# Kernel tuning notes

Measured on AMD Instinct MI355X. Metric: run time of the kernel, lower is better.

## Reference

```python
import jax, jax.numpy as jnp
import numpy as np

TOPK = 5

def _l2norm(x, axis):
    n = jnp.sqrt(jnp.sum(x * x, axis=axis, keepdims=True))
    return x / jnp.maximum(n, 1e-12)

def _conv_block(x, w, b, g, beta):
    # Conv2d(k=3, stride=2, pad=1) + BatchNorm (train-mode batch stats) + ReLU + AvgPool2d(3,1,pad=1)
    x = jax.lax.conv_general_dilated(x, w, (2, 2), ((1, 1), (1, 1)),
                                     dimension_numbers=('NCHW', 'OIHW', 'NCHW'))
    x = x + b[None, :, None, None]
    mean = jnp.mean(x, axis=(0, 2, 3), keepdims=True)
    var = jnp.mean((x - mean) ** 2, axis=(0, 2, 3), keepdims=True)
    x = (x - mean) * jax.lax.rsqrt(var + 1e-5) * g[None, :, None, None] + beta[None, :, None, None]
    x = jax.nn.relu(x)
    # AvgPool2d default count_include_pad=True -> always divide by 9
    x = jax.lax.reduce_window(x, 0.0, jax.lax.add, (1, 1, 3, 3), (1, 1, 1, 1),
                              ((0, 0), (0, 0), (1, 1), (1, 1))) / 9.0
    return x

def _encode(x, params):
    x = x[:, None]  # B,1,T,D
    for (w, b, g, beta) in params:
        x = _conv_block(x, w, b, g, beta)
    return jnp.mean(x, axis=(2, 3))  # AdaptiveAvgPool2d(1) + flatten

def setup_inputs() -> dict:
    key = jax.random.key(0)
    ks = jax.random.split(key, 8)
    B, T, D = 128, 1024, 128
    dim, capQ, refD = 128, 2048, 2304
    inp = {}
    inp['feats'] = jax.random.normal(ks[0], (B, 2, T, D), jnp.float32)
    inp['ref_feats'] = jax.random.normal(ks[1], (B, refD), jnp.float32)
    inp['indices'] = jax.random.randint(ks[2], (B,), 0, 10000)
    mq = jax.random.normal(ks[3], (dim, capQ), jnp.float32)
    inp['MoCoQueue'] = mq / jnp.maximum(jnp.linalg.norm(mq, axis=0, keepdims=True), 1e-12)
    rq = jax.random.normal(ks[4], (refD, capQ), jnp.float32)
    inp['RefQueue'] = rq / jnp.maximum(jnp.linalg.norm(rq, axis=0, keepdims=True), 1e-12)
    inp['IndexQueue'] = jax.random.randint(ks[5], (capQ,), 0, 10000).astype(jnp.float32)
    chans = [1, 4, 16, 64, 128]
    pk = jax.random.split(ks[6], 4)
    for i in range(4):
        ci, co = chans[i], chans[i + 1]
        inp['w%d' % (i + 1)] = jax.random.normal(pk[i], (co, ci, 3, 3), jnp.float32) * 0.1
        inp['b%d' % (i + 1)] = jnp.zeros((co,), jnp.float32)
        inp['g%d' % (i + 1)] = jnp.ones((co,), jnp.float32)
        inp['be%d' % (i + 1)] = jnp.zeros((co,), jnp.float32)
    return inp

def reference(feats, ref_feats, indices, MoCoQueue, RefQueue, IndexQueue,
              w1, b1, g1, be1, w2, b2, g2, be2, w3, b3, g3, be3, w4, b4, g4, be4):
    params = [(w1, b1, g1, be1), (w2, b2, g2, be2), (w3, b3, g3, be3), (w4, b4, g4, be4)]
    q = _l2norm(_encode(feats[:, 1], params), 1)                      # B,dim
    k = jax.lax.stop_gradient(_l2norm(_encode(feats[:, 0], params), 1))
    ref = _l2norm(ref_feats, 1)                                       # B,2304
    B = q.shape[0]
    score_pos = jnp.sum(q * k, axis=1, keepdims=True)                 # B,1
    score_neg = q @ jax.lax.stop_gradient(MoCoQueue)                  # B,capQ
    mask = indices[:, None].astype(IndexQueue.dtype) == IndexQueue[None, :]  # B,capQ bool
    # queue_full=True branch: topk over reference queue similarities + scatter reweighting
    score_ref = ref @ jax.lax.stop_gradient(RefQueue)                 # B,capQ
    masked = jnp.where(mask, -jnp.inf, score_ref)
    _, idx = jax.lax.top_k(masked, TOPK)                              # B,topK
    score_ref2 = jnp.where(mask, 1.0, score_ref)
    rows = jnp.arange(B)[:, None]
    weighted = jnp.full_like(score_neg, -1.0).at[rows, idx].set(1.0)
    mask_f = mask.astype(jnp.float32).at[rows, idx].set(1.0)
    score_neg = score_neg * score_ref2 * weighted
    score = jnp.concatenate([score_pos, score_neg], axis=1)           # B,1+capQ
    mask_out = jnp.concatenate([jnp.ones((B, 1), jnp.float32), mask_f], axis=1)
    return score, mask_out
```

## Files before the change

kernel.cpp:

```cpp
#include <hip/hip_runtime.h>


#define NIMG 128
typedef __attribute__((ext_vector_type(8))) short bf16x8;
typedef __attribute__((ext_vector_type(4))) float f32x4;
typedef __attribute__((ext_vector_type(4))) unsigned int u32x4;
typedef unsigned long long ull;

__device__ __forceinline__ unsigned short f2bf(float f) {
  unsigned u = __float_as_uint(f);
  unsigned r = (u + 0x7fffu + ((u >> 16) & 1u)) >> 16;
  return (unsigned short)r;
}
__device__ __forceinline__ float bf2f(unsigned short u) {
  return __uint_as_float((unsigned)u << 16);
}

__global__ __launch_bounds__(256) void wtr4_k(
    const float* __restrict__ w2, const float* __restrict__ w3,
    const float* __restrict__ w4, unsigned short* __restrict__ wb2,
    unsigned short* __restrict__ wb3, unsigned short* __restrict__ wb4) {
  const int i = blockIdx.x * 256 + threadIdx.x;
  if (i < 16 * 64) {
    int co = i / 64, k = i % 64;
    int tap = k >> 2, ci = k & 3;
    float v = (k < 36) ? w2[co * 36 + ci * 9 + tap] : 0.f;
    wb2[i] = f2bf(v);
  }
  if (i < 64 * 160) {
    int co = i / 160, k = i % 160;
    int tap = k >> 4, ci = k & 15;
    float v = (k < 144) ? w3[co * 144 + ci * 9 + tap] : 0.f;
    wb3[i] = f2bf(v);
  }
  if (i < 128 * 576) {
    int co = i / 576, k = i % 576;
    int tap = k / 64, ci = k & 63;
    wb4[i] = f2bf(w4[co * 576 + ci * 9 + tap]);
  }
}

__device__ __forceinline__ void l1row(const float* __restrict__ ib, int ih,
                                      int w0i, float* r) {
  if (ih < 0) {
#pragma unroll
    for (int q = 0; q < 9; ++q) r[q] = 0.f;
    return;
  }
  const float* rp = ib + ih * 128 + 2 * w0i;
  const float4 a = *(const float4*)rp;
  const float4 b = *(const float4*)(rp + 4);
  r[0] = (w0i > 0) ? rp[-1] : 0.f;
  r[1] = a.x; r[2] = a.y; r[3] = a.z; r[4] = a.w;
  r[5] = b.x; r[6] = b.y; r[7] = b.z; r[8] = b.w;
}

__global__ __launch_bounds__(256, 4) void conv1s_k(const float* __restrict__ feats,
    const float* __restrict__ w1, const float* __restrict__ b1,
    unsigned short* __restrict__ y, float* __restrict__ part1,
    float* __restrict__ part2) {
  constexpr int TH = 2;
  const int tid = threadIdx.x;
  const int lw = tid & 15, grp = tid >> 4;
  const int h0 = (blockIdx.x * 16 + grp) * TH;
  const int pn = blockIdx.z;
  const int p = pn >> 7, n = pn & 127;
  const int sel = (p == 0) ? 1 : 0;
  const float* ib = feats + (size_t)(n * 2 + sel) * 131072;
  const int w0i = lw * 4;

  float wgt[36];
#pragma unroll
  for (int t = 0; t < 36; ++t) wgt[t] = w1[t];
  float bv[4];
#pragma unroll
  for (int c = 0; c < 4; ++c) bv[c] = b1[c];

  float r[5][9];
#pragma unroll
  for (int j = 0; j < 5; ++j) l1row(ib, 2 * h0 - 1 + j, w0i, r[j]);

  float s1[4] = {0.f, 0.f, 0.f, 0.f}, s2[4] = {0.f, 0.f, 0.f, 0.f};
#pragma unroll
  for (int t = 0; t < TH; ++t) {
    const int h = h0 + t;
    const float* r0 = r[2 * t];
    const float* r1 = r[2 * t + 1];
    const float* r2 = r[2 * t + 2];
#pragma unroll
    for (int co = 0; co < 4; ++co) {
      unsigned short ob[4];
#pragma unroll
      for (int i = 0; i < 4; ++i) {
        float v = bv[co];
#pragma unroll
        for (int kw = 0; kw < 3; ++kw) {
          v = fmaf(wgt[co * 9 + kw],     r0[2 * i + kw], v);
          v = fmaf(wgt[co * 9 + 3 + kw], r1[2 * i + kw], v);
          v = fmaf(wgt[co * 9 + 6 + kw], r2[2 * i + kw], v);
        }
        ob[i] = f2bf(v);
        s1[co] += v; s2[co] += v * v;
      }
      const ull o = (ull)ob[0] | ((ull)ob[1] << 16) | ((ull)ob[2] << 32)
                  | ((ull)ob[3] << 48);
      *(ull*)(y + (((size_t)pn * 4 + co) * 512 + h) * 64 + w0i) = o;
    }
  }
  __shared__ float ws1[4][4], ws2[4][4];
  const int lane = tid & 63, wid = tid >> 6;
#pragma unroll
  for (int co = 0; co < 4; ++co) {
#pragma unroll
    for (int m = 32; m >= 1; m >>= 1) {
      s1[co] += __shfl_xor(s1[co], m);
      s2[co] += __shfl_xor(s2[co], m);
    }
    if (lane == 0) { ws1[wid][co] = s1[co]; ws2[wid][co] = s2[co]; }
  }
  __syncthreads();
  if (tid < 4) {
    const float t1 = ws1[0][tid] + ws1[1][tid] + ws1[2][tid] + ws1[3][tid];
    const float t2 = ws2[0][tid] + ws2[1][tid] + ws2[2][tid] + ws2[3][tid];
    const int nblk = gridDim.x * 128;
    const int blk = (pn & 127) * gridDim.x + blockIdx.x;
    part1[(size_t)(p * 4 + tid) * nblk + blk] = t1;
    part2[(size_t)(p * 4 + tid) * nblk + blk] = t2;
  }
}

__device__ __forceinline__ bf16x8 ld16z(const unsigned short* p, bool ok) {
  u32x4 v = *(const u32x4*)p;
  if (!ok) v = (u32x4){0u, 0u, 0u, 0u};
  union { u32x4 a; bf16x8 b; } u; u.a = v; return u.b;
}

template<int Cin, int H, int W, int M, int SPB, int KP, int WCO, int WSP,
         int Cout, int MSPLIT, int WAVES>
__global__ __launch_bounds__(256, WAVES) void cgemmr_k(
    const unsigned short* __restrict__ x,
    const unsigned short* __restrict__ wb,
    const float* __restrict__ bias, unsigned short* __restrict__ y,
    float* __restrict__ part1, float* __restrict__ part2) {
  constexpr int Ho = H / 2, Wo = W / 2, HWout = Ho * Wo;
  constexpr int lgWo = (Wo == 8 ? 3 : (Wo == 16 ? 4 : 5));
  constexpr int lgCin = (Cin == 4 ? 2 : (Cin == 16 ? 4 : 6));
  constexpr int MB = M / MSPLIT;
  constexpr int MT = WCO / 16, NT = WSP / 16, KS = KP / 32;
  constexpr int NWN = SPB / WSP;
  __shared__ float ss1[MB], ss2[MB];
  const int tid = threadIdx.x;
  const int pnl = blockIdx.y;
  const int p = pnl >> 7;
  const int spc = blockIdx.x / MSPLIT;
  const int mc = blockIdx.x - spc * MSPLIT;
  const int sp0 = spc * SPB;
  const int m0 = mc * MB;
  const int lane = tid & 63, wid = tid >> 6;
  const int wm = wid / NWN, wn = wid - wm * NWN;
  const int l15 = lane & 15, lg = lane >> 4;
  const unsigned short* xb = x + (size_t)pnl * Cin * (H * W);

  for (int i = tid; i < MB; i += 256) { ss1[i] = 0.f; ss2[i] = 0.f; }
  __syncthreads();

  int ihb[NT], iwb[NT];
#pragma unroll
  for (int nt = 0; nt < NT; ++nt) {
    const int sp = sp0 + wn * WSP + nt * 16 + l15;
    ihb[nt] = 2 * (sp >> lgWo) - 1;
    iwb[nt] = 2 * (sp & (Wo - 1)) - 1;
  }

  f32x4 acc[MT][NT];
#pragma unroll
  for (int mt = 0; mt < MT; ++mt)
#pragma unroll
    for (int nt = 0; nt < NT; ++nt) acc[mt][nt] = (f32x4){0.f, 0.f, 0.f, 0.f};

#pragma unroll
  for (int ks = 0; ks < KS; ++ks) {
    const int kbase = ks * 32 + lg * 8;
    bf16x8 af[MT];
#pragma unroll
    for (int mt = 0; mt < MT; ++mt)
      af[mt] = *(const bf16x8*)(wb + (size_t)(m0 + wm * WCO + mt * 16 + l15) * KP
                                + kbase);
    bf16x8 bfr[NT];
#pragma unroll
    for (int nt = 0; nt < NT; ++nt) {
      if constexpr (Cin >= 8) {
        const int tap = kbase >> lgCin;
        const int ci0 = kbase & (Cin - 1);
        const int kh = tap / 3, kw = tap - kh * 3;
        const int ih = ihb[nt] + kh, iw = iwb[nt] + kw;
        const bool ok = (tap < 9) & ((unsigned)ih < (unsigned)H)
                      & ((unsigned)iw < (unsigned)W);
        const int off = ok ? ((ih * W + iw) * Cin + ci0) : 0;
        bfr[nt] = ld16z(xb + off, ok);
      } else {
        ull hv[2];
#pragma unroll
        for (int hh = 0; hh < 2; ++hh) {
          const int tap = (kbase >> 2) + hh;
          const int kh = tap / 3, kw = tap - kh * 3;
          const int ih = ihb[nt] + kh, iw = iwb[nt] + kw;
          const bool ok = (tap < 9) & ((unsigned)ih < (unsigned)H)
                        & ((unsigned)iw < (unsigned)W);
          const int off = ok ? ((ih * W + iw) * 4) : 0;
          const ull v = *(const ull*)(xb + off);
          hv[hh] = ok ? v : 0ull;
        }
        union { ull u[2]; bf16x8 b; } uu;
        uu.u[0] = hv[0]; uu.u[1] = hv[1];
        bfr[nt] = uu.b;
      }
    }
#pragma unroll
    for (int mt = 0; mt < MT; ++mt)
#pragma unroll
      for (int nt = 0; nt < NT; ++nt)
        acc[mt][nt] = __builtin_amdgcn_mfma_f32_16x16x32_bf16(af[mt], bfr[nt], acc[mt][nt], 0, 0, 0);
  }

  unsigned short* yb = y + (size_t)pnl * Cout * HWout;
#pragma unroll
  for (int mt = 0; mt < MT; ++mt) {
#pragma unroll
    for (int i = 0; i < 4; ++i) {
      const int col = wm * WCO + mt * 16 + lg * 4 + i;
      const int co = m0 + col;
      const float bv = bias[co];
      float s1 = 0.f, s2 = 0.f;
#pragma unroll
      for (int nt = 0; nt < NT; ++nt) {
        const float v = acc[mt][nt][i] + bv;
        yb[(size_t)co * HWout + sp0 + wn * WSP + nt * 16 + l15] = f2bf(v);
        s1 += v; s2 += v * v;
      }
#pragma unroll
      for (int m = 1; m < 16; m <<= 1) { s1 += __shfl_xor(s1, m); s2 += __shfl_xor(s2, m); }
      if (l15 == 0) {
        atomicAdd(&ss1[col], s1);
        atomicAdd(&ss2[col], s2);
      }
    }
  }
  __syncthreads();
  const int nspc = gridDim.x / MSPLIT;
  const int nblk = nspc * 128;
  const int blkid = (pnl & 127) * nspc + spc;
  for (int i = tid; i < MB; i += 256) {
    part1[(size_t)(p * Cout + m0 + i) * nblk + blkid] = ss1[i];
    part2[(size_t)(p * Cout + m0 + i) * nblk + blkid] = ss2[i];
  }
}

template<int Cin, int H, int W, int M, int SPB, int KP, int KC, int WCO, int WSP,
         int Cout, int MSPLIT>
__global__ __launch_bounds__(256) void cgemmi_k(
    const unsigned short* __restrict__ x,
    const unsigned short* __restrict__ wb,
    const float* __restrict__ bias, unsigned short* __restrict__ y,
    float* __restrict__ part1, float* __restrict__ part2) {
  constexpr int Ho = H / 2, Wo = W / 2, HWout = Ho * Wo;
  constexpr int lgWo = (Wo == 8 ? 3 : (Wo == 16 ? 4 : 5));
  constexpr int lgCin = (Cin == 4 ? 2 : (Cin == 16 ? 4 : 6));
  constexpr int MB = M / MSPLIT;
  constexpr int KCP = KC + 8;
  constexpr int MT = WCO / 16, NT = WSP / 16, KS = KC / 32;
  constexpr int NWN = SPB / WSP;
  constexpr int GR = (Cin < 8) ? 4 : 8;
  __shared__ unsigned short wl[MB][KCP];
  __shared__ unsigned short bl[SPB][KCP];
  __shared__ float ss1[MB], ss2[MB];
  const int tid = threadIdx.x;
  const int pnl = blockIdx.y;
  const int p = pnl >> 7;
  const int spc = blockIdx.x / MSPLIT;
  const int mc = blockIdx.x - spc * MSPLIT;
  const int sp0 = spc * SPB;
  const int m0 = mc * MB;
  const int lane = tid & 63, wid = tid >> 6;
  const int wm = wid / NWN, wn = wid - wm * NWN;
  const int l15 = lane & 15, lg = lane >> 4;
  const unsigned short* xb = x + (size_t)pnl * Cin * (H * W);

  for (int i = tid; i < MB; i += 256) { ss1[i] = 0.f; ss2[i] = 0.f; }

  f32x4 acc[MT][NT];
#pragma unroll
  for (int mt = 0; mt < MT; ++mt)
#pragma unroll
    for (int nt = 0; nt < NT; ++nt) acc[mt][nt] = (f32x4){0.f, 0.f, 0.f, 0.f};

  for (int k0 = 0; k0 < KP; k0 += KC) {
    for (int it = tid; it < SPB * (KC / GR); it += 256) {
      const int row = it / (KC / GR);
      const int rem = it - row * (KC / GR);
      const int k = k0 + rem * GR;
      const int tap = k >> lgCin;
      const int ci0 = k & (Cin - 1);
      const int sp = sp0 + row;
      const int ho = sp >> lgWo, wo = sp & (Wo - 1);
      const int kh = tap / 3, kw = tap - kh * 3;
      const int ih = 2 * ho - 1 + kh, iw = 2 * wo - 1 + kw;
      unsigned short* dst = &bl[row][k - k0];
      if (tap < 9 && (unsigned)ih < (unsigned)H && (unsigned)iw < (unsigned)W) {
        const unsigned short* src = xb + ((size_t)(ih * W + iw) * Cin + ci0);
        if constexpr (GR == 4) {
          *(ull*)dst = *(const ull*)src;
        } else {
          *(u32x4*)dst = *(const u32x4*)src;
        }
      } else {
        *(ull*)dst = 0ull;
        if constexpr (GR == 8) *(ull*)(dst + 4) = 0ull;
      }
    }
    for (int it = tid; it < MB * (KC / 8); it += 256) {
      const int row = it / (KC / 8), seg = it - row * (KC / 8);
      const u32x4 v = *(const u32x4*)(wb + (size_t)(m0 + row) * KP + k0 + seg * 8);
      *(u32x4*)(&wl[row][seg * 8]) = v;
    }
    __syncthreads();
#pragma unroll
    for (int ks = 0; ks < KS; ++ks) {
      bf16x8 af[MT], bfr[NT];
#pragma unroll
      for (int mt = 0; mt < MT; ++mt)
        af[mt] = *(const bf16x8*)(&wl[wm * WCO + mt * 16 + l15][ks * 32 + lg * 8]);
#pragma unroll
      for (int nt = 0; nt < NT; ++nt)
        bfr[nt] = *(const bf16x8*)(&bl[wn * WSP + nt * 16 + l15][ks * 32 + lg * 8]);
#pragma unroll
      for (int mt = 0; mt < MT; ++mt)
#pragma unroll
        for (int nt = 0; nt < NT; ++nt)
          acc[mt][nt] = __builtin_amdgcn_mfma_f32_16x16x32_bf16(af[mt], bfr[nt], acc[mt][nt], 0, 0, 0);
    }
    __syncthreads();
  }

  unsigned short* yb = y + (size_t)pnl * Cout * HWout;
#pragma unroll
  for (int mt = 0; mt < MT; ++mt) {
#pragma unroll
    for (int i = 0; i < 4; ++i) {
      const int col = wm * WCO + mt * 16 + lg * 4 + i;
      const int co = m0 + col;
      const float bv = bias[co];
      float s1 = 0.f, s2 = 0.f;
#pragma unroll
      for (int nt = 0; nt < NT; ++nt) {
        const float v = acc[mt][nt][i] + bv;
        yb[(size_t)co * HWout + sp0 + wn * WSP + nt * 16 + l15] = f2bf(v);
        s1 += v; s2 += v * v;
      }
#pragma unroll
      for (int m = 1; m < 16; m <<= 1) { s1 += __shfl_xor(s1, m); s2 += __shfl_xor(s2, m); }
      if (l15 == 0) {
        atomicAdd(&ss1[col], s1);
        atomicAdd(&ss2[col], s2);
      }
    }
  }
  __syncthreads();
  const int nspc = gridDim.x / MSPLIT;
  const int nblk = nspc * 128;
  const int blkid = (pnl & 127) * nspc + spc;
  for (int i = tid; i < MB; i += 256) {
    part1[(size_t)(p * Cout + m0 + i) * nblk + blkid] = ss1[i];
    part2[(size_t)(p * Cout + m0 + i) * nblk + blkid] = ss2[i];
  }
}

__global__ __launch_bounds__(256) void redstat_k(const float* __restrict__ p1,
    const float* __restrict__ p2, float* __restrict__ st, int nblk) {
  const int row = blockIdx.x;
  float s1 = 0.f, s2 = 0.f;
  for (int i = threadIdx.x; i < nblk; i += 256) {
    s1 += p1[(size_t)row * nblk + i];
    s2 += p2[(size_t)row * nblk + i];
  }
  __shared__ float r1[256], r2[256];
  r1[threadIdx.x] = s1; r2[threadIdx.x] = s2;
  __syncthreads();
  for (int stp = 128; stp > 0; stp >>= 1) {
    if (threadIdx.x < stp) {
      r1[threadIdx.x] += r1[threadIdx.x + stp];
      r2[threadIdx.x] += r2[threadIdx.x + stp];
    }
    __syncthreads();
  }
  if (threadIdx.x == 0) {
    st[row] = r1[0];
    st[256 + row] = r2[0];
  }
}

template<int W>
__device__ __forceinline__ void row_hs(const unsigned short* __restrict__ yp,
                                       int hh, int H, int w0, float a, float b,
                                       float* hs) {
  if ((unsigned)hh >= (unsigned)H) { hs[0] = hs[1] = hs[2] = hs[3] = 0.f; return; }
  const unsigned short* rp = yp + hh * W;
  const ull B = *(const ull*)(rp + w0);
  float r0 = 0.f, r5 = 0.f;
  if (w0 > 0) r0 = fmaxf(fmaf(a, bf2f(rp[w0 - 1]), b), 0.f);
  if (w0 + 4 < W) r5 = fmaxf(fmaf(a, bf2f(rp[w0 + 4]), b), 0.f);
  const float r1 = fmaxf(fmaf(a, bf2f((unsigned short)(B & 0xffff)), b), 0.f);
  const float r2 = fmaxf(fmaf(a, bf2f((unsigned short)((B >> 16) & 0xffff)), b), 0.f);
  const float r3 = fmaxf(fmaf(a, bf2f((unsigned short)((B >> 32) & 0xffff)), b), 0.f);
  const float r4 = fmaxf(fmaf(a, bf2f((unsigned short)(B >> 48)), b), 0.f);
  hs[0] = r0 + r1 + r2;
  hs[1] = r1 + r2 + r3;
  hs[2] = r2 + r3 + r4;
  hs[3] = r3 + r4 + r5;
}

template<int Cout, int H, int W>
__global__ __launch_bounds__(256) void bnpool7_k(const unsigned short* __restrict__ y,
    const float* __restrict__ st, const float* __restrict__ g,
    const float* __restrict__ be, unsigned short* __restrict__ x4, float invCnt) {
  constexpr int W4 = W / 4;
  constexpr int lgW4 = (W4 == 16 ? 4 : (W4 == 8 ? 3 : 2));
  constexpr int NCG = Cout / 4;
  constexpr int lgNCG = (NCG == 1 ? 0 : (NCG == 4 ? 2 : 4));
  constexpr int HQ = 256 >> (lgW4 + lgNCG);
  constexpr int TH = 4;
  constexpr int R = HQ * TH;
  constexpr int RS = W * Cout;
  constexpr int RSP = RS + 8;
  constexpr int HW = H * W;
  __shared__ unsigned short lbuf[R * RSP];
  const int tid = threadIdx.x;
  const int wq = tid & (W4 - 1);
  const int cg = (tid >> lgW4) & (NCG - 1);
  const int hq = tid >> (lgW4 + lgNCG);
  const int w0 = wq * 4;
  const int c0 = cg * 4;
  const int h0 = blockIdx.x * R;
  const int ht0 = h0 + hq * TH;
  const int pn = blockIdx.z;
  const int p = pn >> 7;

  float a[4], b[4];
#pragma unroll
  for (int j = 0; j < 4; ++j) {
    const int c = c0 + j;
    const float mean = st[p * Cout + c] * invCnt;
    const float var = fmaxf(st[256 + p * Cout + c] * invCnt - mean * mean, 0.f);
    a[j] = g[c] * rsqrtf(var + 1e-5f);
    b[j] = be[c] - mean * a[j];
  }
  const unsigned short* yb = y + (size_t)pn * Cout * (size_t)HW;

  float hsA[4][4], hsB[4][4], hsC[4][4];
#pragma unroll
  for (int j = 0; j < 4; ++j)
    row_hs<W>(yb + (size_t)(c0 + j) * HW, ht0 - 1, H, w0, a[j], b[j], hsA[j]);
#pragma unroll
  for (int j = 0; j < 4; ++j)
    row_hs<W>(yb + (size_t)(c0 + j) * HW, ht0, H, w0, a[j], b[j], hsB[j]);
#pragma unroll
  for (int t = 0; t < TH; ++t) {
    const int h = ht0 + t;
    const int lh = hq * TH + t;
#pragma unroll
    for (int j = 0; j < 4; ++j)
      row_hs<W>(yb + (size_t)(c0 + j) * HW, h + 1, H, w0, a[j], b[j], hsC[j]);
#pragma unroll
    for (int i = 0; i < 4; ++i) {
      unsigned short ob[4];
#pragma unroll
      for (int j = 0; j < 4; ++j)
        ob[j] = f2bf((hsA[j][i] + hsB[j][i] + hsC[j][i]) * (1.f / 9.f));
      const ull o = (ull)ob[0] | ((ull)ob[1] << 16) | ((ull)ob[2] << 32)
                  | ((ull)ob[3] << 48);
      *(ull*)(&lbuf[lh * RSP + (w0 + i) * Cout + c0]) = o;
    }
#pragma unroll
    for (int j = 0; j < 4; ++j)
#pragma unroll
      for (int i = 0; i < 4; ++i) { hsA[j][i] = hsB[j][i]; hsB[j][i] = hsC[j][i]; }
  }
  __syncthreads();
  unsigned short* xp = x4 + ((size_t)pn * HW + (size_t)h0 * W) * Cout;
  constexpr int SEGS = RS / 8;
  for (int it = tid; it < R * SEGS; it += 256) {
    const int row = it / SEGS, seg = it - row * SEGS;
    const u32x4 v = *(const u32x4*)(&lbuf[row * RSP + seg * 8]);
    *(u32x4*)(xp + (size_t)row * RS + seg * 8) = v;
  }
}

template<int Cout, int H, int W, int TH>
__global__ __launch_bounds__(256) void bnpool3_k(const unsigned short* __restrict__ y,
    const float* __restrict__ st, const float* __restrict__ g,
    const float* __restrict__ be, unsigned short* __restrict__ x, float invCnt) {
  constexpr int W4 = W / 4;
  constexpr int GROUPS = 256 / W4;
  constexpr int HW = H * W;
  const int tid = threadIdx.x;
  const int grp = tid / W4, lw = tid - grp * W4;
  const int w0 = lw * 4;
  const int h0 = (blockIdx.x * GROUPS + grp) * TH;
  if (h0 >= H) return;
  const int pn = blockIdx.z, c = blockIdx.y;
  const int p = pn >> 7;
  const float mean = st[p * Cout + c] * invCnt;
  const float var = fmaxf(st[256 + p * Cout + c] * invCnt - mean * mean, 0.f);
  const float a = g[c] * rsqrtf(var + 1e-5f);
  const float b = be[c] - mean * a;
  const unsigned short* yp = y + ((size_t)pn * Cout + c) * (size_t)HW;
  unsigned short* xp = x + ((size_t)pn * Cout + c) * (size_t)HW;

  float hsA[4], hsB[4], hsC[4];
  row_hs<W>(yp, h0 - 1, H, w0, a, b, hsA);
  row_hs<W>(yp, h0, H, w0, a, b, hsB);
#pragma unroll
  for (int t = 0; t < TH; ++t) {
    const int h = h0 + t;
    if (h >= H) break;
    row_hs<W>(yp, h + 1, H, w0, a, b, hsC);
    const ull o = (ull)f2bf((hsA[0] + hsB[0] + hsC[0]) * (1.f / 9.f))
                | ((ull)f2bf((hsA[1] + hsB[1] + hsC[1]) * (1.f / 9.f)) << 16)
                | ((ull)f2bf((hsA[2] + hsB[2] + hsC[2]) * (1.f / 9.f)) << 32)
                | ((ull)f2bf((hsA[3] + hsB[3] + hsC[3]) * (1.f / 9.f)) << 48);
    *(ull*)(xp + h * W + w0) = o;
#pragma unroll
    for (int i = 0; i < 4; ++i) { hsA[i] = hsB[i]; hsB[i] = hsC[i]; }
  }
}

__global__ __launch_bounds__(256) void feat2_k(const unsigned short* __restrict__ x,
    float* __restrict__ qk, float* __restrict__ qkT) {
  const int pn = blockIdx.x;
  const int tid = threadIdx.x;
  const int lane = tid & 63, wid = tid >> 6;
  __shared__ float fm[128];
  __shared__ float red[128];
  const unsigned short* xb = x + (size_t)pn * 128 * 512;
  for (int c = wid; c < 128; c += 4) {
    const unsigned short* xp = xb + (size_t)c * 512;
    float s = 0.f;
#pragma unroll
    for (int r = 0; r < 4; ++r) {
      const unsigned v = *(const unsigned*)(xp + lane * 2 + r * 128);
      s += bf2f((unsigned short)(v & 0xffff)) + bf2f((unsigned short)(v >> 16));
    }
#pragma unroll
    for (int m = 32; m >= 1; m >>= 1) s += __shfl_xor(s, m);
    if (lane == 0) fm[c] = s * (1.f / 512.f);
  }
  __syncthreads();
  if (tid < 128) red[tid] = fm[tid] * fm[tid];
  __syncthreads();
  for (int step = 64; step > 0; step >>= 1) {
    if (tid < step) red[tid] += red[tid + step];
    __syncthreads();
  }
  const float inv = 1.f / fmaxf(sqrtf(red[0]), 1e-12f);
  if (tid < 128) {
    const float v = fm[tid] * inv;
    qk[(size_t)pn * 128 + tid] = v;
    if (pn < 128) qkT[(size_t)tid * 128 + pn] = v;
  }
}

__global__ __launch_bounds__(256) void refnorm_k(const float* __restrict__ rf,
    float* __restrict__ rinv) {
  const int n = blockIdx.x;
  float s = 0.f;
  for (int i = threadIdx.x; i < 2304; i += 256) {
    float v = rf[(size_t)n * 2304 + i];
    s += v * v;
  }
  __shared__ float red[256];
  red[threadIdx.x] = s;
  __syncthreads();
  for (int step = 128; step > 0; step >>= 1) {
    if (threadIdx.x < step) red[threadIdx.x] += red[threadIdx.x + step];
    __syncthreads();
  }
  if (threadIdx.x == 0) rinv[n] = 1.f / fmaxf(sqrtf(red[0]), 1e-12f);
}

__global__ __launch_bounds__(256) void reft_k(const float* __restrict__ rf,
    const float* __restrict__ rinv, float* __restrict__ rfT) {
  const int flat = blockIdx.x * 256 + threadIdx.x;
  const int n = flat / 2304, k = flat - n * 2304;
  rfT[(size_t)k * 128 + n] = rf[flat] * rinv[n];
}

__global__ __launch_bounds__(256) void sneg2_k(const float* __restrict__ qkT,
    const float* __restrict__ moco, float* __restrict__ out) {
  const int j = blockIdx.x * 256 + threadIdx.x;
  const int n0 = blockIdx.y * 8;
  float acc[8] = {0.f};
#pragma unroll 4
  for (int k = 0; k < 128; ++k) {
    const float rv = moco[(size_t)k * 2048 + j];
    const float* qp = qkT + (size_t)k * 128 + n0;
#pragma unroll
    for (int i = 0; i < 8; ++i) acc[i] = fmaf(qp[i], rv, acc[i]);
  }
#pragma unroll
  for (int i = 0; i < 8; ++i) out[(size_t)(n0 + i) * 2048 + j] = acc[i];
}

template<int KCH>
__global__ __launch_bounds__(256) void sref3_k(const float* __restrict__ rfT,
    const float* __restrict__ rq, float* __restrict__ part) {
  const int j = blockIdx.x * 256 + threadIdx.x;
  const int n0 = blockIdx.y * 8;
  const int kc = blockIdx.z;
  const int kbeg = kc * KCH;
  float acc[8] = {0.f};
#pragma unroll 4
  for (int k = kbeg; k < kbeg + KCH; ++k) {
    const float rv = rq[(size_t)k * 2048 + j];
    const float* rp = rfT + (size_t)k * 128 + n0;
#pragma unroll
    for (int i = 0; i < 8; ++i) acc[i] = fmaf(rp[i], rv, acc[i]);
  }
  float* pb = part + (size_t)kc * (128 * 2048);
#pragma unroll
  for (int i = 0; i < 8; ++i) pb[(size_t)(n0 + i) * 2048 + j] = acc[i];
}

template<int NCH>
__global__ __launch_bounds__(256) void sredr_k(const float* __restrict__ part,
    float* __restrict__ out) {
  const int j = blockIdx.x * 256 + threadIdx.x;
  const int n = blockIdx.y;
  const size_t off = (size_t)n * 2048 + j;
  float s = 0.f;
#pragma unroll
  for (int c = 0; c < NCH; ++c) s += part[(size_t)c * (128 * 2048) + off];
  out[off] = s;
}

__global__ __launch_bounds__(256) void topk_k(const float* __restrict__ sref,
    const float* __restrict__ iq, const int* __restrict__ idxs,
    int* __restrict__ top) {
  const int n = blockIdx.x;
  const float target = (float)idxs[n];
  float vals[8];
#pragma unroll
  for (int r = 0; r < 8; ++r) {
    const int j = threadIdx.x + r * 256;
    const bool m = (iq[j] == target);
    vals[r] = m ? -__builtin_inff() : sref[(size_t)n * 2048 + j];
  }
  __shared__ float sv[256];
  __shared__ int si[256];
  __shared__ int chosen[5];
  for (int rnd = 0; rnd < 5; ++rnd) {
    float bv = -__builtin_inff();
    int bi = 1 << 30;
#pragma unroll
    for (int r = 0; r < 8; ++r) {
      const int j = threadIdx.x + r * 256;
      bool taken = false;
      for (int t = 0; t < rnd; ++t) taken |= (chosen[t] == j);
      const float v = vals[r];
      if (!taken && (v > bv || (v == bv && j < bi))) { bv = v; bi = j; }
    }
    sv[threadIdx.x] = bv; si[threadIdx.x] = bi;
    __syncthreads();
    for (int step = 128; step > 0; step >>= 1) {
      if (threadIdx.x < step) {
        const float ov = sv[threadIdx.x + step];
        const int oi = si[threadIdx.x + step];
        if (ov > sv[threadIdx.x] || (ov == sv[threadIdx.x] && oi < si[threadIdx.x])) {
          sv[threadIdx.x] = ov; si[threadIdx.x] = oi;
        }
      }
      __syncthreads();
    }
    if (threadIdx.x == 0) chosen[rnd] = si[0];
    __syncthreads();
  }
  if (threadIdx.x < 5) top[n * 5 + threadIdx.x] = chosen[threadIdx.x];
}

__global__ __launch_bounds__(128) void spos_k(const float* __restrict__ qk,
    float* __restrict__ out) {
  const int n = threadIdx.x;
  float s = 0.f;
  for (int c = 0; c < 128; ++c)
    s = fmaf(qk[(size_t)n * 128 + c], qk[(size_t)(NIMG + n) * 128 + c], s);
  out[(size_t)n * 2049] = s;
  out[(size_t)NIMG * 2049 + (size_t)n * 2049] = 1.f;
}

__global__ __launch_bounds__(256) void asm_k(const float* __restrict__ sneg,
    const float* __restrict__ sref, const float* __restrict__ iq,
    const int* __restrict__ idxs, const int* __restrict__ top,
    float* __restrict__ out) {
  const int n = blockIdx.y;
  const int j = blockIdx.x * 256 + threadIdx.x;
  const int t0 = top[n * 5 + 0], t1 = top[n * 5 + 1], t2 = top[n * 5 + 2];
  const int t3 = top[n * 5 + 3], t4 = top[n * 5 + 4];
  const float target = (float)idxs[n];
  const bool m = (iq[j] == target);
  const float sr = sref[(size_t)n * 2048 + j];
  const float sr2 = m ? 1.f : sr;
  const bool istop = (j == t0) | (j == t1) | (j == t2) | (j == t3) | (j == t4);
  const float wgt = istop ? 1.f : -1.f;
  out[(size_t)n * 2049 + 1 + j] = sneg[(size_t)n * 2048 + j] * sr2 * wgt;
  const float mf = istop ? 1.f : (m ? 1.f : 0.f);
  out[(size_t)NIMG * 2049 + (size_t)n * 2049 + 1 + j] = mf;
}

extern "C" void kernel_launch(void* const* d_in, const int* in_sizes, int n_in,
                              void* d_out, int out_size, void* d_ws, size_t ws_size,
                              hipStream_t stream) {
  const float* feats = (const float*)d_in[0];
  const float* reff  = (const float*)d_in[1];
  const int*   idxs  = (const int*)d_in[2];
  const float* moco  = (const float*)d_in[3];
  const float* refq  = (const float*)d_in[4];
  const float* iq    = (const float*)d_in[5];
  const float* w[4]  = {(const float*)d_in[6],  (const float*)d_in[10],
                        (const float*)d_in[14], (const float*)d_in[18]};
  const float* b[4]  = {(const float*)d_in[7],  (const float*)d_in[11],
                        (const float*)d_in[15], (const float*)d_in[19]};
  const float* g[4]  = {(const float*)d_in[8],  (const float*)d_in[12],
                        (const float*)d_in[16], (const float*)d_in[20]};
  const float* be[4] = {(const float*)d_in[9],  (const float*)d_in[13],
                        (const float*)d_in[17], (const float*)d_in[21]};
  float* out = (float*)d_out;

  const size_t BIG = 33554432;
  unsigned short* X = (unsigned short*)d_ws;
  unsigned short* Y = X + BIG;
  float* ST   = (float*)(Y + BIG);
  unsigned short* WB2 = (unsigned short*)(ST + 2048);
  unsigned short* WB3 = WB2 + 1024;
  unsigned short* WB4 = WB3 + 10240;
  float* QK   = (float*)(WB4 + 73728);
  float* QKT  = QK + 32768;
  float* RINV = QKT + 16384;
  float* RFT  = RINV + 128;
  float* SNEG = RFT + 294912;
  float* SREF = SNEG + 262144;
  int*   TOP  = (int*)(SREF + 262144);
  float* SPART = (float*)(TOP + 256);
  unsigned short* X4 = (unsigned short*)(SPART + 6 * 128 * 2048);
  float* PART1 = SNEG;
  float* PART2 = SNEG + 131072;

  wtr4_k<<<288, 256, 0, stream>>>(w[1], w[2], w[3], WB2, WB3, WB4);

  conv1s_k<<<dim3(16, 1, 256), 256, 0, stream>>>(feats, w[0], b[0], Y, PART1, PART2);
  redstat_k<<<8, 256, 0, stream>>>(PART1, PART2, ST, 2048);
  bnpool7_k<4, 512, 64><<<dim3(8, 1, 256), 256, 0, stream>>>(Y, ST, g[0], be[0], X4,
                                                             1.f / (128.f * 32768.f));
  cgemmr_k<4, 512, 64, 16, 256, 64, 16, 64, 16, 1, 6>
      <<<dim3(32, 256), 256, 0, stream>>>(X4, WB2, b[1], Y, PART1, PART2);
  redstat_k<<<32, 256, 0, stream>>>(PART1, PART2, ST + 512, 32 * 128);
  bnpool7_k<16, 256, 32><<<dim3(8, 1, 256), 256, 0, stream>>>(Y, ST + 512, g[1], be[1], X4,
                                                              1.f / (128.f * 8192.f));
  cgemmr_k<16, 256, 32, 64, 256, 160, 64, 64, 64, 1, 3>
      <<<dim3(8, 256), 256, 0, stream>>>(X4, WB3, b[2], Y, PART1, PART2);
  redstat_k<<<128, 256, 0, stream>>>(PART1, PART2, ST + 1024, 8 * 128);
  bnpool7_k<64, 128, 16><<<dim3(8, 1, 256), 256, 0, stream>>>(Y, ST + 1024, g[2], be[2], X4,
                                                              1.f / (128.f * 2048.f));
  cgemmi_k<64, 128, 16, 128, 128, 576, 64, 32, 64, 128, 2>
      <<<dim3(8, 256), 256, 0, stream>>>(X4, WB4, b[3], Y, PART1, PART2);
  redstat_k<<<256, 256, 0, stream>>>(PART1, PART2, ST + 1536, 4 * 128);
  bnpool3_k<128, 64, 8, 1><<<dim3(1, 128, 256), 256, 0, stream>>>(Y, ST + 1536, g[3], be[3], X,
                                                                  1.f / (128.f * 512.f));

  feat2_k<<<256, 256, 0, stream>>>(X, QK, QKT);
  refnorm_k<<<128, 256, 0, stream>>>(reff, RINV);
  reft_k<<<1152, 256, 0, stream>>>(reff, RINV, RFT);
  sneg2_k<<<dim3(8, 16), 256, 0, stream>>>(QKT, moco, SNEG);
  sref3_k<384><<<dim3(8, 16, 6), 256, 0, stream>>>(RFT, refq, SPART);
  sredr_k<6><<<dim3(8, 128), 256, 0, stream>>>(SPART, SREF);
  topk_k<<<128, 256, 0, stream>>>(SREF, iq, idxs, TOP);
  spos_k<<<1, 128, 0, stream>>>(QK, out);
  asm_k<<<dim3(8, 128), 256, 0, stream>>>(SNEG, SREF, iq, idxs, TOP, out);
}
```

Measured before the change: 530.7 us.

## Fold final BN+avgpool into global mean via border coverage weights; reorder loads

Replaces the last bnpool3 kernel and the feature-mean kernel with one kernel that applies BN+ReLU and computes the spatial mean directly. Each pixel is weighted by how many 3x3 pool windows cover it (2 or 3 per axis). This removes a full write and re-read of the pooled bf16 activation plus one launch. It also moves the weight tile load ahead of the im2col gather in the conv GEMM loop. Rounding changes slightly because the pooled tensor is no longer stored as bf16.

New measurement: 483.9 us. 8.8% less time.

```diff
diff --git a/kernel.cpp b/kernel.cpp
--- a/kernel.cpp
+++ b/kernel.cpp
@@ -295,6 +295,11 @@
     for (int nt = 0; nt < NT; ++nt) acc[mt][nt] = (f32x4){0.f, 0.f, 0.f, 0.f};
 
   for (int k0 = 0; k0 < KP; k0 += KC) {
+    for (int it = tid; it < MB * (KC / 8); it += 256) {
+      const int row = it / (KC / 8), seg = it - row * (KC / 8);
+      const u32x4 v = *(const u32x4*)(wb + (size_t)(m0 + row) * KP + k0 + seg * 8);
+      *(u32x4*)(&wl[row][seg * 8]) = v;
+    }
     for (int it = tid; it < SPB * (KC / GR); it += 256) {
       const int row = it / (KC / GR);
       const int rem = it - row * (KC / GR);
@@ -317,11 +322,6 @@
         *(ull*)dst = 0ull;
         if constexpr (GR == 8) *(ull*)(dst + 4) = 0ull;
       }
-    }
-    for (int it = tid; it < MB * (KC / 8); it += 256) {
-      const int row = it / (KC / 8), seg = it - row * (KC / 8);
-      const u32x4 v = *(const u32x4*)(wb + (size_t)(m0 + row) * KP + k0 + seg * 8);
-      *(u32x4*)(&wl[row][seg * 8]) = v;
     }
     __syncthreads();
 #pragma unroll
@@ -495,64 +495,42 @@
   }
 }
 
-template<int Cout, int H, int W, int TH>
-__global__ __launch_bounds__(256) void bnpool3_k(const unsigned short* __restrict__ y,
+__global__ __launch_bounds__(256) void feat3_k(const unsigned short* __restrict__ y,
     const float* __restrict__ st, const float* __restrict__ g,
-    const float* __restrict__ be, unsigned short* __restrict__ x, float invCnt) {
-  constexpr int W4 = W / 4;
-  constexpr int GROUPS = 256 / W4;
-  constexpr int HW = H * W;
-  const int tid = threadIdx.x;
-  const int grp = tid / W4, lw = tid - grp * W4;
-  const int w0 = lw * 4;
-  const int h0 = (blockIdx.x * GROUPS + grp) * TH;
-  if (h0 >= H) return;
-  const int pn = blockIdx.z, c = blockIdx.y;
+    const float* __restrict__ be, float* __restrict__ qk, float* __restrict__ qkT) {
+  const int pn = blockIdx.x;
   const int p = pn >> 7;
-  const float mean = st[p * Cout + c] * invCnt;
-  const float var = fmaxf(st[256 + p * Cout + c] * invCnt - mean * mean, 0.f);
-  const float a = g[c] * rsqrtf(var + 1e-5f);
-  const float b = be[c] - mean * a;
-  const unsigned short* yp = y + ((size_t)pn * Cout + c) * (size_t)HW;
-  unsigned short* xp = x + ((size_t)pn * Cout + c) * (size_t)HW;
-
-  float hsA[4], hsB[4], hsC[4];
-  row_hs<W>(yp, h0 - 1, H, w0, a, b, hsA);
-  row_hs<W>(yp, h0, H, w0, a, b, hsB);
-#pragma unroll
-  for (int t = 0; t < TH; ++t) {
-    const int h = h0 + t;
-    if (h >= H) break;
-    row_hs<W>(yp, h + 1, H, w0, a, b, hsC);
-    const ull o = (ull)f2bf((hsA[0] + hsB[0] + hsC[0]) * (1.f / 9.f))
-                | ((ull)f2bf((hsA[1] + hsB[1] + hsC[1]) * (1.f / 9.f)) << 16)
-                | ((ull)f2bf((hsA[2] + hsB[2] + hsC[2]) * (1.f / 9.f)) << 32)
-                | ((ull)f2bf((hsA[3] + hsB[3] + hsC[3]) * (1.f / 9.f)) << 48);
-    *(ull*)(xp + h * W + w0) = o;
-#pragma unroll
-    for (int i = 0; i < 4; ++i) { hsA[i] = hsB[i]; hsB[i] = hsC[i]; }
-  }
-}
-
-__global__ __launch_bounds__(256) void feat2_k(const unsigned short* __restrict__ x,
-    float* __restrict__ qk, float* __restrict__ qkT) {
-  const int pn = blockIdx.x;
   const int tid = threadIdx.x;
   const int lane = tid & 63, wid = tid >> 6;
   __shared__ float fm[128];
   __shared__ float red[128];
-  const unsigned short* xb = x + (size_t)pn * 128 * 512;
+  const unsigned short* yb = y + (size_t)pn * 128 * 512;
+  const float invCnt = 1.f / (128.f * 512.f);
   for (int c = wid; c < 128; c += 4) {
-    const unsigned short* xp = xb + (size_t)c * 512;
+    const float mean = st[p * 128 + c] * invCnt;
+    const float var = fmaxf(st[256 + p * 128 + c] * invCnt - mean * mean, 0.f);
+    const float a = g[c] * rsqrtf(var + 1e-5f);
+    const float b = be[c] - mean * a;
+    const unsigned short* yp = yb + (size_t)c * 512;
     float s = 0.f;
 #pragma unroll
     for (int r = 0; r < 4; ++r) {
-      const unsigned v = *(const unsigned*)(xp + lane * 2 + r * 128);
-      s += bf2f((unsigned short)(v & 0xffff)) + bf2f((unsigned short)(v >> 16));
+      const int pos0 = lane * 2 + r * 128;
+      const unsigned v = *(const unsigned*)(yp + pos0);
+#pragma unroll
+      for (int e = 0; e < 2; ++e) {
+        const int pos = pos0 + e;
+        const int h = pos >> 3, w = pos & 7;
+        const float cov = ((h == 0 || h == 63) ? 2.f : 3.f)
+                        * ((w == 0 || w == 7) ? 2.f : 3.f);
+        const unsigned short u = (e == 0) ? (unsigned short)(v & 0xffff)
+                                          : (unsigned short)(v >> 16);
+        s += fmaxf(fmaf(a, bf2f(u), b), 0.f) * cov;
+      }
     }
 #pragma unroll
     for (int m = 32; m >= 1; m >>= 1) s += __shfl_xor(s, m);
-    if (lane == 0) fm[c] = s * (1.f / 512.f);
+    if (lane == 0) fm[c] = s * (1.f / (9.f * 512.f));
   }
   __syncthreads();
   if (tid < 128) red[tid] = fm[tid] * fm[tid];
@@ -772,10 +750,8 @@
   cgemmi_k<64, 128, 16, 128, 128, 576, 64, 32, 64, 128, 2>
       <<<dim3(8, 256), 256, 0, stream>>>(X4, WB4, b[3], Y, PART1, PART2);
   redstat_k<<<256, 256, 0, stream>>>(PART1, PART2, ST + 1536, 4 * 128);
-  bnpool3_k<128, 64, 8, 1><<<dim3(1, 128, 256), 256, 0, stream>>>(Y, ST + 1536, g[3], be[3], X,
-                                                                  1.f / (128.f * 512.f));
-
-  feat2_k<<<256, 256, 0, stream>>>(X, QK, QKT);
+
+  feat3_k<<<256, 256, 0, stream>>>(Y, ST + 1536, g[3], be[3], QK, QKT);
   refnorm_k<<<128, 256, 0, stream>>>(reff, RINV);
   reft_k<<<1152, 256, 0, stream>>>(reff, RINV, RFT);
   sneg2_k<<<dim3(8, 16), 256, 0, stream>>>(QKT, moco, SNEG);
```
